# Kernel tuning notes

Measured on AMD Instinct MI355X. Metric: run time of the kernel, lower is better.

The kernel has to match this reference:

```python
import jax, jax.numpy as jnp
import numpy as np

V = 32000; EMB = 128; EH = 256; DH = 256; AD = 256; BN = 512
UNK, START, END, PAD = 0, 1, 2, 3
COV_FACTOR = 1.0
B, T_IN, T_TGT = 16, 400, 100


def _lstm_cell(x, h, c, Wih, Whh, b):
    # PyTorch gate order: i, f, g, o
    g = x @ Wih.T + h @ Whh.T + b
    i, f, gg, o = jnp.split(g, 4, axis=-1)
    c = jax.nn.sigmoid(f) * c + jax.nn.sigmoid(i) * jnp.tanh(gg)
    h = jax.nn.sigmoid(o) * jnp.tanh(c)
    return h, c


def _lstm_scan(xs, Wih, Whh, b):
    # xs: [T, B, Din]
    Bz, H = xs.shape[1], Whh.shape[-1]
    def step(carry, xt):
        h, c = _lstm_cell(xt, carry[0], carry[1], Wih, Whh, b)
        return (h, c), h
    init = (jnp.zeros((Bz, H), xs.dtype), jnp.zeros((Bz, H), xs.dtype))
    (hT, cT), hs = jax.lax.scan(step, init, xs)
    return hs, hT, cT


def _bilstm(x, Wih, Whh, b):
    # x: [B, T, Din]; Wih/Whh/b stacked over direction (fwd, bwd)
    xs = jnp.swapaxes(x, 0, 1)
    hf, hTf, cTf = _lstm_scan(xs, Wih[0], Whh[0], b[0])
    hb, hTb, cTb = _lstm_scan(xs[::-1], Wih[1], Whh[1], b[1])
    out = jnp.concatenate([hf, hb[::-1]], axis=-1)  # [T, B, 2H]
    return jnp.swapaxes(out, 0, 1), jnp.concatenate([hTf, hTb], -1), jnp.concatenate([cTf, cTb], -1)


def forward_loss(emb, enc_Wih0, enc_Whh0, enc_b0, enc_Wih1, enc_Whh1, enc_b1, W_e2dh, b_e2dh, W_e2dc, b_e2dc, dec_Wih0, dec_Whh0, dec_b0, dec_Wih1, dec_Whh1, dec_b1, W_enc_attn, b_enc_attn, W_dec_attn, w_cov, v_attn, W_v1, b_v1, W_v2, b_v2, w_ctx_sw, b_ctx_sw, w_dec_sw, w_emb_sw, input_ids, target_ids, target_lengths):
    Bz, Tt = target_ids.shape
    safe_in = jnp.where(input_ids >= V, UNK, input_ids)
    x0 = emb[safe_in]                                          # [B, T_in, EMB]
    h_seq, hT0, cT0 = _bilstm(x0, enc_Wih0, enc_Whh0, enc_b0)
    enc_states, hT1, cT1 = _bilstm(h_seq, enc_Wih1, enc_Whh1, enc_b1)  # [B, T_in, 2*EH]
    hT = jnp.stack([hT0, hT1])                                 # [2, B, 2*EH] (fwd||bwd per layer)
    cT = jnp.stack([cT0, cT1])
    dec_h = hT @ W_e2dh.T + b_e2dh                             # [2, B, DH]
    dec_c = cT @ W_e2dc.T + b_e2dc
    enc_attn = enc_states @ W_enc_attn.T + b_enc_attn          # precomputed, loop-invariant
    pad_mask = input_ids == PAD
    safe_tgt = jnp.where(target_ids >= V, UNK, target_ids)
    # teacher forcing: input at t=0 is <s>, then safe(target[t-1])
    tok_in = jnp.concatenate([jnp.full((Bz, 1), START, dtype=target_ids.dtype), safe_tgt[:, :-1]], axis=1)

    def step(carry, inp):
        dh, dc, coverage, nll, cov = carry
        tok_t, tgt_t, t = inp
        e = emb[tok_t]
        h0, c0 = _lstm_cell(e, dh[0], dc[0], dec_Wih0, dec_Whh0, dec_b0)
        h1, c1 = _lstm_cell(h0, dh[1], dc[1], dec_Wih1, dec_Whh1, dec_b1)
        feat = jnp.tanh(enc_attn + (h1 @ W_dec_attn.T)[:, None, :] + coverage[..., None] * w_cov)
        scores = jnp.where(pad_mask, -jnp.inf, feat @ v_attn)
        attn = jax.nn.softmax(scores, axis=1)                  # [B, T_in]
        ctx = jnp.einsum('bt,btd->bd', attn, enc_states)
        vd = jax.nn.softmax(jax.nn.relu(jnp.concatenate([h1, ctx], axis=1) @ W_v1.T + b_v1) @ W_v2.T + b_v2, axis=1)
        # extended vocab = END left-pad zeros + generation dist (max_num_oovs = 0)
        p_vocab = jnp.take_along_axis(jnp.pad(vd, ((0, 0), (END, 0))), tgt_t[:, None], axis=1)[:, 0]
        p_gen = jax.nn.sigmoid(ctx @ w_ctx_sw + b_ctx_sw[0] + h1 @ w_dec_sw + e @ w_emb_sw)
        p_copy = jnp.sum(attn * (input_ids == tgt_t[:, None]), axis=1)
        p = p_gen * p_vocab + (1.0 - p_gen) * p_copy
        active = t < target_lengths
        nll = nll - jnp.where(active, jnp.log(p + 1e-9), 0.0)
        cov = cov + jnp.where(active, jnp.sum(jnp.minimum(attn, coverage), axis=1), 0.0)
        return (jnp.stack([h0, h1]), jnp.stack([c0, c1]), coverage + attn, nll, cov), None

    init = (dec_h, dec_c, jnp.zeros(input_ids.shape, enc_states.dtype), jnp.zeros((Bz,), enc_states.dtype), jnp.zeros((Bz,), enc_states.dtype))
    (_, _, _, nll, cov), _ = jax.lax.scan(step, init, (tok_in.T, target_ids.T, jnp.arange(Tt)))
    nll_loss = nll.sum()
    cov_loss = cov.sum()
    return jnp.stack([nll_loss, cov_loss, nll_loss + COV_FACTOR * cov_loss])


def setup_inputs() -> dict:
    ks = iter(jax.random.split(jax.random.key(0), 48))
    def w(shape, scale=0.05):
        return (jax.random.normal(next(ks), shape) * scale).astype(jnp.float32)
    def lstm_b(*shape):
        b = np.zeros(shape, np.float32)
        n = shape[-1]
        b[..., n // 4: n // 2] = 1.0  # forget-gate bias = 1 as in init_weights
        return jnp.asarray(b)
    inp = {}
    inp['batch_input_ids'] = jax.random.randint(next(ks), (B, T_IN), 0, V)
    inp['batch_target_ids'] = jax.random.randint(next(ks), (B, T_TGT), 0, V)
    inp['input_lengths'] = jnp.full((B,), T_IN, dtype=jnp.int32)  # full-length batch
    inp['target_lengths'] = jax.random.randint(next(ks), (B,), 1, T_TGT + 1)
    inp['emb'] = w((V, EMB), 0.1)
    inp['enc_Wih0'] = w((2, 4 * EH, EMB)); inp['enc_Whh0'] = w((2, 4 * EH, EH)); inp['enc_b0'] = lstm_b(2, 4 * EH)
    inp['enc_Wih1'] = w((2, 4 * EH, 2 * EH)); inp['enc_Whh1'] = w((2, 4 * EH, EH)); inp['enc_b1'] = lstm_b(2, 4 * EH)
    inp['W_e2dh'] = w((DH, 2 * EH)); inp['b_e2dh'] = jnp.zeros((DH,), jnp.float32)
    inp['W_e2dc'] = w((DH, 2 * EH)); inp['b_e2dc'] = jnp.zeros((DH,), jnp.float32)
    inp['dec_Wih0'] = w((4 * DH, EMB)); inp['dec_Whh0'] = w((4 * DH, DH)); inp['dec_b0'] = lstm_b(4 * DH)
    inp['dec_Wih1'] = w((4 * DH, DH)); inp['dec_Whh1'] = w((4 * DH, DH)); inp['dec_b1'] = lstm_b(4 * DH)
    inp['W_enc_attn'] = w((AD, 2 * EH)); inp['b_enc_attn'] = jnp.zeros((AD,), jnp.float32)
    inp['W_dec_attn'] = w((AD, DH))
    inp['w_cov'] = w((AD,))
    inp['v_attn'] = w((AD,))
    inp['W_v1'] = w((BN, DH + 2 * EH)); inp['b_v1'] = jnp.zeros((BN,), jnp.float32)
    inp['W_v2'] = w((V - END, BN)); inp['b_v2'] = jnp.zeros((V - END,), jnp.float32)
    inp['w_ctx_sw'] = w((2 * EH,)); inp['b_ctx_sw'] = jnp.zeros((1,), jnp.float32)
    inp['w_dec_sw'] = w((DH,)); inp['w_emb_sw'] = w((EMB,))
    return inp


def reference(batch_input_ids, batch_target_ids, input_lengths, target_lengths, emb, enc_Wih0, enc_Whh0, enc_b0, enc_Wih1, enc_Whh1, enc_b1, W_e2dh, b_e2dh, W_e2dc, b_e2dc, dec_Wih0, dec_Whh0, dec_b0, dec_Wih1, dec_Whh1, dec_b1, W_enc_attn, b_enc_attn, W_dec_attn, w_cov, v_attn, W_v1, b_v1, W_v2, b_v2, w_ctx_sw, b_ctx_sw, w_dec_sw, w_emb_sw):
    del input_lengths  # all sequences are full length -> pack/pad_packed is identity
    return forward_loss(emb, enc_Wih0, enc_Whh0, enc_b0, enc_Wih1, enc_Whh1, enc_b1, W_e2dh, b_e2dh, W_e2dc, b_e2dc, dec_Wih0, dec_Whh0, dec_b0, dec_Wih1, dec_Whh1, dec_b1, W_enc_attn, b_enc_attn, W_dec_attn, w_cov, v_attn, W_v1, b_v1, W_v2, b_v2, w_ctx_sw, b_ctx_sw, w_dec_sw, w_emb_sw, batch_input_ids, batch_target_ids, target_lengths)
```

## Files before the change

### kernel.cpp

```cpp
#include <hip/hip_runtime.h>
#include <hip/hip_bf16.h>

#define B    16
#define TIN  400
#define TT   100
#define EMBD 128
#define VV   32000
#define NV   31998
#define NVB  192
#define NB   256
#define LR   112
#define REP  8

__device__ __forceinline__ float sigf(float x) { return 1.f / (1.f + __expf(-x)); }
__device__ __forceinline__ float fast_tanh(float x) {
    float e = __expf(2.f * x);
    return 1.f - 2.f / (e + 1.f);
}
__device__ __forceinline__ float bflo(unsigned u) { return __uint_as_float(u << 16); }
__device__ __forceinline__ float bfhi(unsigned u) { return __uint_as_float(u & 0xffff0000u); }
__device__ __forceinline__ float bfu(unsigned short u) { return __uint_as_float((unsigned)u << 16); }
__device__ __forceinline__ unsigned short f2bf(float f) {
    unsigned u = __float_as_uint(f);
    return (unsigned short)((u + 0x7fffu + ((u >> 16) & 1u)) >> 16);
}
__device__ __forceinline__ float cldf(const float* p) {
    return __hip_atomic_load(p, __ATOMIC_RELAXED, __HIP_MEMORY_SCOPE_AGENT);
}
__device__ __forceinline__ unsigned cldu(const unsigned* p) {
    return __hip_atomic_load(p, __ATOMIC_RELAXED, __HIP_MEMORY_SCOPE_AGENT);
}
__device__ __forceinline__ unsigned long long cldu2(const unsigned long long* p) {
    return __hip_atomic_load(p, __ATOMIC_RELAXED, __HIP_MEMORY_SCOPE_AGENT);
}
__device__ __forceinline__ void stf(float* p, float v) {
    __hip_atomic_store(p, v, __ATOMIC_RELAXED, __HIP_MEMORY_SCOPE_AGENT);
}
__device__ __forceinline__ void stu(unsigned* p, unsigned v) {
    __hip_atomic_store(p, v, __ATOMIC_RELAXED, __HIP_MEMORY_SCOPE_AGENT);
}

template<int SLP>
__device__ __forceinline__ void wait_np(int* arr, int n, int ep, int tid) {
    for (int i = tid; i < n; i += 256) {
        while (__hip_atomic_load(&arr[i * 16], __ATOMIC_RELAXED, __HIP_MEMORY_SCOPE_AGENT) < ep)
            __builtin_amdgcn_s_sleep(SLP);
    }
    __syncthreads();
    asm volatile("" ::: "memory");
}
template<int SLP>
__device__ __forceinline__ void wait_line(int* l, int ep) {
    if (threadIdx.x == 0) {
        while (__hip_atomic_load(l, __ATOMIC_RELAXED, __HIP_MEMORY_SCOPE_AGENT) < ep)
            __builtin_amdgcn_s_sleep(SLP);
    }
    __syncthreads();
    asm volatile("" ::: "memory");
}
__device__ __forceinline__ void arrive(int* arr, int idx, int ep) {
    __syncthreads();
    if (threadIdx.x == 0)
        __hip_atomic_store(&arr[idx * 16], ep, __ATOMIC_RELEASE, __HIP_MEMORY_SCOPE_AGENT);
}

__global__ __launch_bounds__(256) void k_zero(float* __restrict__ p, int n) {
    int i = blockIdx.x * 256 + threadIdx.x;
    if (i < n) p[i] = 0.f;
}

__global__ __launch_bounds__(256) void k_cvt(const float* __restrict__ src, unsigned short* __restrict__ dst, int n) {
    int i = blockIdx.x * 256 + threadIdx.x;
    if (i < n) dst[i] = f2bf(src[i]);
}

__global__ __launch_bounds__(256) void k_gx0(const int* __restrict__ ids, const float* __restrict__ emb,
                                             const float* __restrict__ Wih, const float* __restrict__ bias,
                                             float* __restrict__ gx) {
    int blk = blockIdx.x, dir = blk / TIN, t = blk % TIN;
    __shared__ float se[16][132];
    int tid = threadIdx.x;
    for (int i = tid; i < 16 * 128; i += 256) {
        int b = i >> 7, k = i & 127;
        int id = ids[b * TIN + t];
        if ((unsigned)id >= VV) id = 0;
        se[b][k] = emb[(size_t)id * EMBD + k];
    }
    __syncthreads();
    const float* W = Wih + (size_t)dir * 1024 * EMBD;
    const float* bb = bias + (size_t)dir * 1024;
    float* out = gx + ((size_t)dir * TIN + t) * (B * 1024);
    for (int c = tid; c < 1024; c += 256) {
        float acc[16];
#pragma unroll
        for (int b = 0; b < 16; b++) acc[b] = 0.f;
        const float4* wr = (const float4*)(W + (size_t)c * EMBD);
        for (int k4 = 0; k4 < 32; k4++) {
            float4 w = wr[k4];
            int k = k4 * 4;
#pragma unroll
            for (int b = 0; b < 16; b++)
                acc[b] += w.x * se[b][k] + w.y * se[b][k + 1] + w.z * se[b][k + 2] + w.w * se[b][k + 3];
        }
        float bv = bb[c];
#pragma unroll
        for (int b = 0; b < 16; b++) out[(size_t)b * 1024 + c] = acc[b] + bv;
    }
}

__global__ __launch_bounds__(256) void k_gx1(const float* __restrict__ hseq, const float* __restrict__ Wih,
                                             const float* __restrict__ bias, float* __restrict__ gx) {
    int blk = blockIdx.x, dir = blk / TIN, t = blk % TIN;
    __shared__ float sx[16][516];
    int tid = threadIdx.x;
    for (int i = tid; i < 16 * 512; i += 256) sx[i >> 9][i & 511] = hseq[(size_t)t * B * 512 + i];
    __syncthreads();
    const float* W = Wih + (size_t)dir * 1024 * 512;
    const float* bb = bias + (size_t)dir * 1024;
    float* out = gx + ((size_t)dir * TIN + t) * (B * 1024);
    for (int c = tid; c < 1024; c += 256) {
        float acc[16];
#pragma unroll
        for (int b = 0; b < 16; b++) acc[b] = 0.f;
        const float4* wr = (const float4*)(W + (size_t)c * 512);
        for (int k4 = 0; k4 < 128; k4++) {
            float4 w = wr[k4];
            int k = k4 * 4;
#pragma unroll
            for (int b = 0; b < 16; b++)
                acc[b] += w.x * sx[b][k] + w.y * sx[b][k + 1] + w.z * sx[b][k + 2] + w.w * sx[b][k + 3];
        }
        float bv = bb[c];
#pragma unroll
        for (int b = 0; b < 16; b++) out[(size_t)b * 1024 + c] = acc[b] + bv;
    }
}

__global__ __launch_bounds__(256) void k_enc_layer(const float* __restrict__ gx, const float* __restrict__ Whh,
                                                   float* __restrict__ hbuf, float* __restrict__ hout,
                                                   float* __restrict__ hTs, float* __restrict__ cTs,
                                                   int* __restrict__ slots, int layer) {
    int blk = blockIdx.x;
    int dir = blk >> 4;
    int ublk = blk & 15;
    int tid = threadIdx.x;
    int rp = tid >> 3, q = tid & 7;
    int lr0 = rp * 2, lr1 = lr0 + 1;
    int g0 = lr0 & 3, g1 = lr1 & 3;
    int unit0 = ublk * 16 + (lr0 >> 2);
    int unit1 = ublk * 16 + (lr1 >> 2);
    const float* Wd = Whh + (size_t)dir * 1024 * 256;
    float wreg[64];
    {
        const float* r0 = Wd + (size_t)(g0 * 256 + unit0) * 256 + q * 32;
        const float* r1 = Wd + (size_t)(g1 * 256 + unit1) * 256 + q * 32;
#pragma unroll
        for (int e = 0; e < 32; e++) { wreg[e] = r0[e]; wreg[32 + e] = r1[e]; }
    }
    int ub = tid >> 4, bb = tid & 15;
    float creg = 0.f;
    __shared__ float sh[16 * 288];
    __shared__ float sums[32 * 17];
    __shared__ float sums2[32 * 17];
    int* dirslots = slots + (size_t)dir * TIN * 16 * 16;

    for (int s = 0; s < TIN; s++) {
        int t = dir ? (TIN - 1 - s) : s;
        int par = s & 1;
        {
            const unsigned long long* hp = (const unsigned long long*)(hbuf + ((size_t)par * 2 + dir) * B * 256);
            unsigned long long v[8];
#pragma unroll
            for (int j = 0; j < 8; j++) v[j] = cldu2(hp + tid + 256 * j);
#pragma unroll
            for (int j = 0; j < 8; j++) {
                int k2 = (tid + 256 * j) * 2;
                int b = k2 >> 8, k = k2 & 255;
                float* d = &sh[b * 288 + (k >> 5) * 36 + (k & 31)];
                d[0] = __uint_as_float((unsigned)v[j]);
                d[1] = __uint_as_float((unsigned)(v[j] >> 32));
            }
        }
        __syncthreads();
        float pa0[16], pa1[16];
        for (int b = 0; b < 16; b++) {
            const float4* hv = (const float4*)&sh[b * 288 + q * 36];
            float a0 = 0.f, a1 = 0.f;
#pragma unroll
            for (int j = 0; j < 8; j++) {
                float4 h4 = hv[j];
                a0 += wreg[4 * j] * h4.x + wreg[4 * j + 1] * h4.y + wreg[4 * j + 2] * h4.z + wreg[4 * j + 3] * h4.w;
                a1 += wreg[32 + 4 * j] * h4.x + wreg[33 + 4 * j] * h4.y + wreg[34 + 4 * j] * h4.z + wreg[35 + 4 * j] * h4.w;
            }
            pa0[b] = a0; pa1[b] = a1;
        }
#pragma unroll
        for (int m = 1; m < 8; m <<= 1) {
#pragma unroll
            for (int b = 0; b < 16; b++) {
                pa0[b] += __shfl_xor(pa0[b], m, 64);
                pa1[b] += __shfl_xor(pa1[b], m, 64);
            }
        }
        if (q == 0) {
            float* s0 = (lr0 < 32) ? sums : sums2;
            float* s1 = (lr1 < 32) ? sums : sums2;
            int l0 = lr0 & 31, l1 = lr1 & 31;
#pragma unroll
            for (int b = 0; b < 16; b++) { s0[l0 * 17 + b] = pa0[b]; s1[l1 * 17 + b] = pa1[b]; }
        }
        __syncthreads();
        {
            int unit = ublk * 16 + ub;
            const float* gp = gx + (((size_t)dir * TIN + t) * B + bb) * 1024;
            int lri = ub * 4;
            float ai = ((lri + 0 < 32) ? sums[(lri + 0) * 17 + bb] : sums2[((lri + 0) & 31) * 17 + bb]) + gp[0 * 256 + unit];
            float af = ((lri + 1 < 32) ? sums[(lri + 1) * 17 + bb] : sums2[((lri + 1) & 31) * 17 + bb]) + gp[1 * 256 + unit];
            float ag = ((lri + 2 < 32) ? sums[(lri + 2) * 17 + bb] : sums2[((lri + 2) & 31) * 17 + bb]) + gp[2 * 256 + unit];
            float ao = ((lri + 3 < 32) ? sums[(lri + 3) * 17 + bb] : sums2[((lri + 3) & 31) * 17 + bb]) + gp[3 * 256 + unit];
            float c = sigf(af) * creg + sigf(ai) * fast_tanh(ag);
            float h = sigf(ao) * fast_tanh(c);
            creg = c;
            stf(&hbuf[((size_t)(par ^ 1) * 2 + dir) * B * 256 + (size_t)bb * 256 + unit], h);
            if (layer == 0) hout[((size_t)t * B + bb) * 512 + dir * 256 + unit] = h;
            else            hout[((size_t)bb * TIN + t) * 512 + dir * 256 + unit] = h;
            if (s == TIN - 1) {
                hTs[((size_t)layer * B + bb) * 512 + dir * 256 + unit] = h;
                cTs[((size_t)layer * B + bb) * 512 + dir * 256 + unit] = c;
            }
        }
        int* sl = dirslots + (size_t)s * 16 * 16;
        arrive(sl, ublk, 1);
        wait_np<2>(sl, 16, 1, tid);
    }
}

__global__ __launch_bounds__(256) void k_encattn(const float* __restrict__ encs, const float* __restrict__ Wea,
                                                 const float* __restrict__ bea, unsigned short* __restrict__ encat) {
    int blk = blockIdx.x;
    __shared__ float sx[8][520];
    int tid = threadIdx.x;
    for (int i = tid; i < 8 * 512; i += 256) {
        int r = i >> 9, k = i & 511;
        sx[r][k] = encs[((size_t)blk * 8 + r) * 512 + k];
    }
    __syncthreads();
    float a[8];
    float bv = bea[tid];
#pragma unroll
    for (int r = 0; r < 8; r++) a[r] = bv;
    const float4* wr = (const float4*)(Wea + (size_t)tid * 512);
    for (int k4 = 0; k4 < 128; k4++) {
        float4 w = wr[k4];
        int k = k4 * 4;
#pragma unroll
        for (int r = 0; r < 8; r++)
            a[r] += w.x * sx[r][k] + w.y * sx[r][k + 1] + w.z * sx[r][k + 2] + w.w * sx[r][k + 3];
    }
#pragma unroll
    for (int r = 0; r < 8; r++)
        encat[((size_t)blk * 8 + r) * 256 + tid] = f2bf(a[r]);
}

__global__ __launch_bounds__(256) void k_dec_init(const float* __restrict__ hTs, const float* __restrict__ cTs,
                                                  const float* __restrict__ Wh, const float* __restrict__ bh,
                                                  const float* __restrict__ Wc, const float* __restrict__ bc,
                                                  float* __restrict__ h0s, float* __restrict__ c0,
                                                  float* __restrict__ h1s, float* __restrict__ c1) {
    int idx = blockIdx.x * 256 + threadIdx.x;
    int l = idx >> 12, b = (idx >> 8) & 15, d = idx & 255;
    const float4* h4 = (const float4*)(hTs + ((size_t)l * B + b) * 512);
    const float4* c4 = (const float4*)(cTs + ((size_t)l * B + b) * 512);
    const float4* wh4 = (const float4*)(Wh + (size_t)d * 512);
    const float4* wc4 = (const float4*)(Wc + (size_t)d * 512);
    float ah = bh[d], ac = bc[d];
    for (int k4 = 0; k4 < 128; k4++) {
        float4 w = wh4[k4], x = h4[k4];
        ah += w.x * x.x + w.y * x.y + w.z * x.z + w.w * x.w;
        w = wc4[k4]; x = c4[k4];
        ac += w.x * x.x + w.y * x.y + w.z * x.z + w.w * x.w;
    }
    if (l == 0) { h0s[(size_t)b * 256 + d] = ah; c0[(size_t)b * 256 + d] = ac; }
    else        { h1s[(size_t)b * 256 + d] = ah; c1[(size_t)b * 256 + d] = ac; }
}

__global__ __launch_bounds__(256, 1) void k_dec_persist(
    const int* __restrict__ ids, const int* __restrict__ tgt, const int* __restrict__ tlen,
    const float* __restrict__ emb,
    const float* __restrict__ dWih0, const float* __restrict__ dWhh0, const float* __restrict__ db0,
    const float* __restrict__ dWih1, const float* __restrict__ dWhh1, const float* __restrict__ db1,
    const float* __restrict__ Wda, const float* __restrict__ wcov, const float* __restrict__ vat,
    const float* __restrict__ Wv1, const float* __restrict__ bv1,
    const unsigned short* __restrict__ W2b, const float* __restrict__ bv2,
    const float* __restrict__ wctx, const float* __restrict__ bctx,
    const float* __restrict__ wdec, const float* __restrict__ wemb,
    const unsigned short* __restrict__ ENCATH, const unsigned short* __restrict__ ENCSH,
    float* __restrict__ COVL,
    unsigned* __restrict__ CTXB, unsigned* __restrict__ FC1B,
    float* __restrict__ PCOPYR, float* __restrict__ VPARTR, float* __restrict__ LTGTR,
    float* __restrict__ H0R, const float* __restrict__ C0i,
    float* __restrict__ H1R, const float* __restrict__ C1i,
    int* __restrict__ SL, float* __restrict__ out)
{
    __shared__ float smem[39040];
    int blk = blockIdx.x, tid = threadIdx.x;
    int* B1 = SL;
    int* B2 = SL + 32 * 16;
    int* B3 = SL + 64 * 16;
    int* B4 = SL + 80 * 16;
    int* SVOC = SL + 96 * 16;
    int* SFRDY = SL + 288 * 16;
    int* FINRDY = SL + 296 * 16;

    if (blk < 32) {
        float creg0 = 0.f, creg1 = 0.f;
        if (tid < 128) {
            creg0 = C0i[(size_t)(tid & 15) * 256 + blk * 8 + (tid >> 4)];
            creg1 = C1i[(size_t)(tid & 15) * 256 + blk * 8 + (tid >> 4)];
        }
        for (int t = 0; t < TT; t++) {
            int ep = t + 1, p8 = t & 7, pm = (t + 7) & 7;
            wait_line<8>(FINRDY, t - 7);
            wait_np<2>(B2, 32, t, tid);

            for (int i = tid; i < 2048; i += 256) {
                int b = i >> 7, k = i & 127;
                int tok = (t == 0) ? 1 : tgt[b * TT + t - 1];
                if ((unsigned)tok >= VV) tok = 0;
                smem[b * 132 + k] = emb[(size_t)tok * 128 + k];
            }
            {
                const unsigned long long* s0 = (const unsigned long long*)(H0R + (size_t)pm * 4096);
                const unsigned long long* s1 = (const unsigned long long*)(H1R + (size_t)pm * 4096);
                unsigned long long v0[8], v1[8];
#pragma unroll
                for (int j = 0; j < 8; j++) v0[j] = cldu2(s0 + tid + 256 * j);
#pragma unroll
                for (int j = 0; j < 8; j++) v1[j] = cldu2(s1 + tid + 256 * j);
#pragma unroll
                for (int j = 0; j < 8; j++) {
                    int k2 = (tid + 256 * j) * 2;
                    int b = k2 >> 8, k = k2 & 255;
                    int off = b * 288 + (k >> 5) * 36 + (k & 31);
                    smem[2112 + off] = __uint_as_float((unsigned)v0[j]);
                    smem[2113 + off] = __uint_as_float((unsigned)(v0[j] >> 32));
                    smem[6720 + off] = __uint_as_float((unsigned)v1[j]);
                    smem[6721 + off] = __uint_as_float((unsigned)(v1[j] >> 32));
                }
            }
            __syncthreads();
            {
                int r = tid >> 3, q = tid & 7;
                int g = r & 3, u = r >> 2;
                int grow = g * 256 + blk * 8 + u;
                float4 wA[4], wB[8];
                const float4* wi4 = (const float4*)(dWih0 + (size_t)grow * 128 + q * 16);
                const float4* wh4 = (const float4*)(dWhh0 + (size_t)grow * 256 + q * 32);
#pragma unroll
                for (int j = 0; j < 4; j++) wA[j] = wi4[j];
#pragma unroll
                for (int j = 0; j < 8; j++) wB[j] = wh4[j];
                float pa[16];
                for (int b = 0; b < 16; b++) {
                    const float4* xe = (const float4*)&smem[b * 132 + q * 16];
                    const float4* xh = (const float4*)&smem[2112 + b * 288 + q * 36];
                    float a = 0.f;
#pragma unroll
                    for (int j = 0; j < 4; j++) { float4 x = xe[j]; a += wA[j].x * x.x + wA[j].y * x.y + wA[j].z * x.z + wA[j].w * x.w; }
#pragma unroll
                    for (int j = 0; j < 8; j++) { float4 x = xh[j]; a += wB[j].x * x.x + wB[j].y * x.y + wB[j].z * x.z + wB[j].w * x.w; }
                    pa[b] = a;
                }
#pragma unroll
                for (int m = 1; m < 8; m <<= 1)
#pragma unroll
                    for (int b = 0; b < 16; b++) pa[b] += __shfl_xor(pa[b], m, 64);
                if (q == 0)
#pragma unroll
                    for (int b = 0; b < 16; b++) smem[11328 + r * 17 + b] = pa[b];
            }
            __syncthreads();
            if (tid < 128) {
                int u = tid >> 4, b = tid & 15;
                int unit = blk * 8 + u;
                float ai = smem[11328 + (u * 4 + 0) * 17 + b] + db0[unit];
                float af = smem[11328 + (u * 4 + 1) * 17 + b] + db0[256 + unit];
                float ag = smem[11328 + (u * 4 + 2) * 17 + b] + db0[512 + unit];
                float ao = smem[11328 + (u * 4 + 3) * 17 + b] + db0[768 + unit];
                float c = sigf(af) * creg0 + sigf(ai) * fast_tanh(ag);
                float h = sigf(ao) * fast_tanh(c);
                creg0 = c;
                stf(&H0R[(size_t)p8 * 4096 + b * 256 + unit], h);
            }
            arrive(B1, blk, ep);
            wait_np<2>(B1, 32, ep, tid);
            {
                const unsigned long long* s0 = (const unsigned long long*)(H0R + (size_t)p8 * 4096);
                unsigned long long v0[8];
#pragma unroll
                for (int j = 0; j < 8; j++) v0[j] = cldu2(s0 + tid + 256 * j);
#pragma unroll
                for (int j = 0; j < 8; j++) {
                    int k2 = (tid + 256 * j) * 2;
                    int b = k2 >> 8, k = k2 & 255;
                    int off = b * 288 + (k >> 5) * 36 + (k & 31);
                    smem[2112 + off] = __uint_as_float((unsigned)v0[j]);
                    smem[2113 + off] = __uint_as_float((unsigned)(v0[j] >> 32));
                }
            }
            __syncthreads();
            {
                int r = tid >> 3, q = tid & 7;
                int g = r & 3, u = r >> 2;
                int grow = g * 256 + blk * 8 + u;
                float4 wA[8], wB[8];
                const float4* wi4 = (const float4*)(dWih1 + (size_t)grow * 256 + q * 32);
                const float4* wh4 = (const float4*)(dWhh1 + (size_t)grow * 256 + q * 32);
#pragma unroll
                for (int j = 0; j < 8; j++) { wA[j] = wi4[j]; wB[j] = wh4[j]; }
                float pa[16];
                for (int b = 0; b < 16; b++) {
                    const float4* xa = (const float4*)&smem[2112 + b * 288 + q * 36];
                    const float4* xb = (const float4*)&smem[6720 + b * 288 + q * 36];
                    float a = 0.f;
#pragma unroll
                    for (int j = 0; j < 8; j++) { float4 x = xa[j]; a += wA[j].x * x.x + wA[j].y * x.y + wA[j].z * x.z + wA[j].w * x.w; }
#pragma unroll
                    for (int j = 0; j < 8; j++) { float4 x = xb[j]; a += wB[j].x * x.x + wB[j].y * x.y + wB[j].z * x.z + wB[j].w * x.w; }
                    pa[b] = a;
                }
#pragma unroll
                for (int m = 1; m < 8; m <<= 1)
#pragma unroll
                    for (int b = 0; b < 16; b++) pa[b] += __shfl_xor(pa[b], m, 64);
                if (q == 0)
#pragma unroll
                    for (int b = 0; b < 16; b++) smem[11328 + r * 17 + b] = pa[b];
            }
            __syncthreads();
            if (tid < 128) {
                int u = tid >> 4, b = tid & 15;
                int unit = blk * 8 + u;
                float ai = smem[11328 + (u * 4 + 0) * 17 + b] + db1[unit];
                float af = smem[11328 + (u * 4 + 1) * 17 + b] + db1[256 + unit];
                float ag = smem[11328 + (u * 4 + 2) * 17 + b] + db1[512 + unit];
                float ao = smem[11328 + (u * 4 + 3) * 17 + b] + db1[768 + unit];
                float c = sigf(af) * creg1 + sigf(ai) * fast_tanh(ag);
                float h = sigf(ao) * fast_tanh(c);
                creg1 = c;
                stf(&H1R[(size_t)p8 * 4096 + b * 256 + unit], h);
            }
            arrive(B2, blk, ep);
        }
    } else if (blk < 48) {
        int b = blk - 32;
        float* sh1 = smem; float* sda = smem + 256; float* ssc = smem + 512;
        float* red = smem + 912; float* sred = smem + 1280; float* scov = smem + 3328;
        for (int i = tid; i < TIN; i += 256) scov[i] = 0.f;
        float covl = 0.f;
        __syncthreads();
        for (int t = 0; t < TT; t++) {
            int ep = t + 1, p8 = t & 7;
            wait_np<2>(B2, 32, ep, tid);
            if (tid < 128) {
                unsigned long long v = cldu2((const unsigned long long*)(H1R + (size_t)p8 * 4096 + b * 256) + tid);
                sh1[2 * tid] = __uint_as_float((unsigned)v);
                sh1[2 * tid + 1] = __uint_as_float((unsigned)(v >> 32));
            }
            __syncthreads();
            {
                float a = 0.f;
                const float4* wr = (const float4*)(Wda + (size_t)tid * 256);
                const float4* h4 = (const float4*)sh1;
                for (int k4 = 0; k4 < 64; k4++) {
                    float4 ww = wr[k4], x = h4[k4];
                    a += ww.x * x.x + ww.y * x.y + ww.z * x.z + ww.w * x.w;
                }
                sda[tid] = a;
            }
            __syncthreads();
            int lane = tid & 63, wv = tid >> 6;
            for (int tt = wv; tt < TIN; tt += 4) {
                float cvv = scov[tt];
                const unsigned short* ea = ENCATH + ((size_t)b * TIN + tt) * 256;
                float s4 = 0.f;
#pragma unroll
                for (int j = 0; j < 4; j++) {
                    int c = lane + 64 * j;
                    float x = bfu(ea[c]) + sda[c] + cvv * wcov[c];
                    s4 += vat[c] * fast_tanh(x);
                }
#pragma unroll
                for (int o = 32; o > 0; o >>= 1) s4 += __shfl_xor(s4, o, 64);
                if (lane == 0) ssc[tt] = (ids[b * TIN + tt] == 3) ? -1e30f : s4;
            }
            __syncthreads();
            float m = -1e30f;
            for (int i = tid; i < TIN; i += 256) m = fmaxf(m, ssc[i]);
            red[tid] = m; __syncthreads();
            for (int o = 128; o > 0; o >>= 1) { if (tid < o) red[tid] = fmaxf(red[tid], red[tid + o]); __syncthreads(); }
            m = red[0]; __syncthreads();
            float ps = 0.f;
            for (int i = tid; i < TIN; i += 256) { float ex = __expf(ssc[i] - m); ssc[i] = ex; ps += ex; }
            red[tid] = ps; __syncthreads();
            for (int o = 128; o > 0; o >>= 1) { if (tid < o) red[tid] += red[tid + o]; __syncthreads(); }
            float inv = 1.f / red[0];
            __syncthreads();
            int tgb = tgt[b * TT + t];
            float pc = 0.f, ca = 0.f;
            for (int i = tid; i < TIN; i += 256) {
                float at = ssc[i] * inv; ssc[i] = at;
                float cv = scov[i];
                ca += fminf(at, cv);
                scov[i] = cv + at;
                if (ids[b * TIN + i] == tgb) pc += at;
            }
            red[tid] = pc; __syncthreads();
            for (int o = 128; o > 0; o >>= 1) { if (tid < o) red[tid] += red[tid + o]; __syncthreads(); }
            if (tid == 0) stf(&PCOPYR[p8 * 16 + b], red[0]);
            __syncthreads();
            red[tid] = ca; __syncthreads();
            for (int o = 128; o > 0; o >>= 1) { if (tid < o) red[tid] += red[tid + o]; __syncthreads(); }
            if (tid == 0 && t < tlen[b]) covl += red[0];
            __syncthreads();
            {
                float acc[8];
#pragma unroll
                for (int j = 0; j < 8; j++) acc[j] = 0.f;
                for (int i = wv; i < TIN; i += 4) {
                    float a = ssc[i];
                    const unsigned short* es = ENCSH + ((size_t)b * TIN + i) * 512;
#pragma unroll
                    for (int j = 0; j < 8; j++) acc[j] += a * bfu(es[lane + 64 * j]);
                }
#pragma unroll
                for (int j = 0; j < 8; j++) sred[wv * 512 + 64 * j + lane] = acc[j];
                __syncthreads();
                {
                    int d2 = tid;
                    float c0 = sred[2 * d2] + sred[512 + 2 * d2] + sred[1024 + 2 * d2] + sred[1536 + 2 * d2];
                    float c1 = sred[2 * d2 + 1] + sred[512 + 2 * d2 + 1] + sred[1024 + 2 * d2 + 1] + sred[1536 + 2 * d2 + 1];
                    unsigned u = (unsigned)f2bf(c0) | ((unsigned)f2bf(c1) << 16);
                    stu(&CTXB[(size_t)p8 * 4096 + b * 256 + d2], u);
                }
            }
            if (t == TT - 1 && tid == 0) stf(&COVL[b], covl);
            arrive(B3, b, ep);
        }
    } else if (blk < 64) {
        int cb = blk - 48;
        float* Wv1s = smem;
        float* x = smem + 24576;
        float* fcout = smem + 36928;
        for (int r = 0; r < 32; r++)
            for (int k = tid; k < 768; k += 256)
                Wv1s[r * 768 + k] = Wv1[(size_t)(cb * 32 + r) * 768 + k];
        __syncthreads();
        for (int t = 0; t < TT; t++) {
            int ep = t + 1, p8 = t & 7;
            wait_np<2>(B3, 16, ep, tid);
            {
                const unsigned long long* s0 = (const unsigned long long*)(H1R + (size_t)p8 * 4096);
                unsigned long long v0[8];
#pragma unroll
                for (int j = 0; j < 8; j++) v0[j] = cldu2(s0 + tid + 256 * j);
#pragma unroll
                for (int j = 0; j < 8; j++) {
                    int k2 = (tid + 256 * j) * 2;
                    int b = k2 >> 8, k = k2 & 255;
                    x[b * 772 + k] = __uint_as_float((unsigned)v0[j]);
                    x[b * 772 + k + 1] = __uint_as_float((unsigned)(v0[j] >> 32));
                }
                const unsigned long long* s1 = (const unsigned long long*)(CTXB + (size_t)p8 * 4096);
                unsigned long long w1[8];
#pragma unroll
                for (int j = 0; j < 8; j++) w1[j] = cldu2(s1 + tid + 256 * j);
#pragma unroll
                for (int j = 0; j < 8; j++) {
                    int g = (tid + 256 * j) * 2;
                    int b = g >> 8, pj = g & 255;
                    unsigned lo = (unsigned)w1[j], hi = (unsigned)(w1[j] >> 32);
                    float* d = &x[b * 772 + 256 + 2 * pj];
                    d[0] = bflo(lo); d[1] = bfhi(lo); d[2] = bflo(hi); d[3] = bfhi(hi);
                }
            }
            __syncthreads();
            {
                int b = tid & 15, cl = tid >> 4;
                const float4* xr = (const float4*)&x[b * 772];
#pragma unroll
                for (int half = 0; half < 2; half++) {
                    int lc = half * 16 + cl;
                    float a = bv1[cb * 32 + lc];
                    const float4* wr = (const float4*)&Wv1s[lc * 768];
                    for (int k4 = 0; k4 < 192; k4++) {
                        float4 ww = wr[k4], xx = xr[k4];
                        a += ww.x * xx.x + ww.y * xx.y + ww.z * xx.z + ww.w * xx.w;
                    }
                    fcout[b * 32 + lc] = fmaxf(a, 0.f);
                }
            }
            __syncthreads();
            {
                int bb = tid >> 4, j = tid & 15;
                unsigned u = (unsigned)f2bf(fcout[bb * 32 + 2 * j]) | ((unsigned)f2bf(fcout[bb * 32 + 2 * j + 1]) << 16);
#pragma unroll
                for (int rp = 0; rp < REP; rp++)
                    stu(&FC1B[((size_t)rp * 8 + p8) * 4096 + bb * 256 + cb * 16 + j], u);
            }
            arrive(B4, cb, ep);
            if (blk == 63) {
                wait_np<2>(B4, 16, ep, tid);
                if (tid == 0) {
#pragma unroll
                    for (int rp = 0; rp < REP; rp++)
                        __hip_atomic_store(&SFRDY[rp * 16], ep, __ATOMIC_RELEASE, __HIP_MEMORY_SCOPE_AGENT);
                }
                __syncthreads();
            }
        }
    } else {
        int vb = blk - 64;
        int start = (int)(((long long)vb * NV) / NVB);
        int end   = (int)(((long long)(vb + 1) * NV) / NVB);
        float* FC1f = smem + 28672;
        float* scratch = smem + 36864;
        uint4* Wl = (uint4*)smem;
        const unsigned* myFC1B = FC1B + (size_t)(vb & 7) * 8 * 4096;
        int* mySF = &SFRDY[(vb & 7) * 16];
        float nllreg = 0.f;
        for (int i = tid; i < LR * 64; i += 256) {
            int row = i >> 6, k8 = i & 63;
            Wl[k8 * LR + row] = *(const uint4*)(W2b + (size_t)(start + row) * 512 + k8 * 8);
        }
        __syncthreads();

        for (int t = 0; t < TT; t++) {
            int ep = t + 1, p8 = t & 7;
            wait_line<4>(mySF, ep);
            {
                const unsigned long long* src = (const unsigned long long*)(myFC1B + (size_t)p8 * 4096);
                unsigned long long v[8];
#pragma unroll
                for (int j = 0; j < 8; j++) v[j] = cldu2(src + tid + 256 * j);
#pragma unroll
                for (int j = 0; j < 8; j++) {
                    int iu = tid + 256 * j;
                    unsigned lo = (unsigned)v[j], hi = (unsigned)(v[j] >> 32);
                    *(float4*)&FC1f[iu * 4] = make_float4(bflo(lo), bfhi(lo), bflo(hi), bfhi(hi));
                }
            }
            __syncthreads();
            int vl = tid & 127, kh = tid >> 7;
            float esum[16];
#pragma unroll
            for (int b = 0; b < 16; b++) esum[b] = 0.f;
            for (int chunk = 0; chunk < 2; chunk++) {
                int v = (chunk == 0) ? (start + vl) : (start + LR + vl);
                bool row_ok = (chunk == 0) ? (vl < LR) : (v < end);
                float acc[16];
#pragma unroll
                for (int b = 0; b < 16; b++) acc[b] = 0.f;
                if (row_ok) {
                    for (int k8l = 0; k8l < 32; k8l++) {
                        int k8 = kh * 32 + k8l;
                        uint4 pw = (chunk == 0) ? Wl[k8 * LR + vl]
                                                : *(const uint4*)(W2b + (size_t)v * 512 + k8 * 8);
                        int k = k8 * 8;
                        float w0 = bflo(pw.x), w1 = bfhi(pw.x);
                        float w2 = bflo(pw.y), w3 = bfhi(pw.y);
                        float w4 = bflo(pw.z), w5 = bfhi(pw.z);
                        float w6 = bflo(pw.w), w7 = bfhi(pw.w);
#pragma unroll
                        for (int b = 0; b < 16; b++) {
                            const float* s = &FC1f[b * 512 + k];
                            acc[b] += w0 * s[0] + w1 * s[1] + w2 * s[2] + w3 * s[3]
                                    + w4 * s[4] + w5 * s[5] + w6 * s[6] + w7 * s[7];
                        }
                    }
                }
                if (kh == 1 && row_ok) {
#pragma unroll
                    for (int b = 0; b < 16; b++) scratch[vl * 17 + b] = acc[b];
                }
                __syncthreads();
                if (kh == 0 && row_ok) {
                    float bias = bv2[v];
#pragma unroll
                    for (int b = 0; b < 16; b++) {
                        float lg = acc[b] + scratch[vl * 17 + b] + bias;
                        if (tgt[b * TT + t] - 2 == v) stf(&LTGTR[p8 * 16 + b], lg);
                        esum[b] += __expf(lg);
                    }
                }
                __syncthreads();
            }
            if (kh == 0) {
#pragma unroll
                for (int b = 0; b < 16; b++) scratch[vl * 17 + b] = esum[b];
            }
            __syncthreads();
            {
                int b = tid >> 4, sl = tid & 15;
                float s = 0.f;
#pragma unroll
                for (int j = 0; j < 8; j++) s += scratch[(sl + 16 * j) * 17 + b];
                FC1f[b * 17 + sl] = s;
            }
            __syncthreads();
            if (tid < 16) {
                float den = 0.f;
#pragma unroll
                for (int j = 0; j < 16; j++) den += FC1f[tid * 17 + j];
                stf(&VPARTR[(size_t)p8 * 3072 + tid * 192 + vb], den);
            }
            __syncthreads();
            arrive(SVOC, vb, ep);

            if (blk == NB - 1) {
                wait_np<2>(SVOC, NVB, ep, tid);
                float* fsc = FC1f;
                int lane = tid & 63, wv = tid >> 6;
                for (int bi = 0; bi < 4; bi++) {
                    int b = wv * 4 + bi;
                    float a = 0.f;
                    for (int k = lane; k < 256; k += 64) {
                        unsigned u = cldu(&CTXB[(size_t)p8 * 4096 + b * 256 + k]);
                        a += bflo(u) * wctx[2 * k] + bfhi(u) * wctx[2 * k + 1];
                    }
                    for (int k = lane; k < 256; k += 64) a += cldf(&H1R[(size_t)p8 * 4096 + b * 256 + k]) * wdec[k];
                    int tok = (t == 0) ? 1 : tgt[b * TT + t - 1];
                    if ((unsigned)tok >= VV) tok = 0;
                    const float* em = emb + (size_t)tok * EMBD;
                    for (int k = lane; k < 128; k += 64) a += em[k] * wemb[k];
#pragma unroll
                    for (int o = 32; o > 0; o >>= 1) a += __shfl_xor(a, o, 64);
                    if (lane == 0) fsc[300 + b] = a;
                }
                {
                    int b = tid >> 4, sl = tid & 15;
                    float s = 0.f;
                    for (int j = sl; j < NVB; j += 16) s += cldf(&VPARTR[(size_t)p8 * 3072 + b * 192 + j]);
                    fsc[b * 17 + sl] = s;
                }
                __syncthreads();
                if (tid < 16) {
                    int b = tid;
                    float den = 0.f;
#pragma unroll
                    for (int j = 0; j < 16; j++) den += fsc[b * 17 + j];
                    float pg = 1.f / (1.f + __expf(-(fsc[300 + b] + bctx[0])));
                    int tg = tgt[b * TT + t];
                    float pv = (tg >= 2) ? (__expf(cldf(&LTGTR[p8 * 16 + b])) / den) : 0.f;
                    float pr = pg * pv + (1.f - pg) * cldf(&PCOPYR[p8 * 16 + b]);
                    if (t < tlen[b]) nllreg += -logf(pr + 1e-9f);
                }
                if (t == TT - 1) {
                    if (tid < 16) fsc[340 + tid] = nllreg;
                    __syncthreads();
                    if (tid == 0) {
                        float sn = 0.f, sc = 0.f;
                        for (int b = 0; b < 16; b++) { sn += fsc[340 + b]; sc += cldf(&COVL[b]); }
                        out[0] = sn; out[1] = sc; out[2] = sn + sc;
                    }
                }
                __syncthreads();
                if (tid == 0)
                    __hip_atomic_store(FINRDY, ep, __ATOMIC_RELEASE, __HIP_MEMORY_SCOPE_AGENT);
            }
        }
    }
}

extern "C" void kernel_launch(void* const* d_in, const int* in_sizes, int n_in,
                              void* d_out, int out_size, void* d_ws, size_t ws_size,
                              hipStream_t stream) {
    (void)in_sizes; (void)n_in; (void)out_size; (void)ws_size;
    const int*   ids   = (const int*)d_in[0];
    const int*   tgt   = (const int*)d_in[1];
    const int*   tlen  = (const int*)d_in[3];
    const float* emb   = (const float*)d_in[4];
    const float* eWih0 = (const float*)d_in[5];
    const float* eWhh0 = (const float*)d_in[6];
    const float* eb0   = (const float*)d_in[7];
    const float* eWih1 = (const float*)d_in[8];
    const float* eWhh1 = (const float*)d_in[9];
    const float* eb1   = (const float*)d_in[10];
    const float* We2dh = (const float*)d_in[11];
    const float* be2dh = (const float*)d_in[12];
    const float* We2dc = (const float*)d_in[13];
    const float* be2dc = (const float*)d_in[14];
    const float* dWih0 = (const float*)d_in[15];
    const float* dWhh0 = (const float*)d_in[16];
    const float* db0   = (const float*)d_in[17];
    const float* dWih1 = (const float*)d_in[18];
    const float* dWhh1 = (const float*)d_in[19];
    const float* db1   = (const float*)d_in[20];
    const float* Wea   = (const float*)d_in[21];
    const float* bea   = (const float*)d_in[22];
    const float* Wda   = (const float*)d_in[23];
    const float* wcov  = (const float*)d_in[24];
    const float* vat   = (const float*)d_in[25];
    const float* Wv1   = (const float*)d_in[26];
    const float* bv1   = (const float*)d_in[27];
    const float* Wv2   = (const float*)d_in[28];
    const float* bv2   = (const float*)d_in[29];
    const float* wctx  = (const float*)d_in[30];
    const float* bctx  = (const float*)d_in[31];
    const float* wdec  = (const float*)d_in[32];
    const float* wemb  = (const float*)d_in[33];
    float* out = (float*)d_out;

    float* ws = (float*)d_ws;
    float* GX    = ws; ws += (size_t)2 * TIN * B * 1024;
    float* HSEQ  = ws; ws += (size_t)TIN * B * 512;
    float* ENCS  = ws; ws += (size_t)B * TIN * 512;
    float* ENCATHf = ws; ws += (size_t)B * TIN * 128;
    float* ENCSHf  = ws; ws += (size_t)B * TIN * 256;
    float* HTS   = ws; ws += 2 * B * 512;
    float* CTS   = ws; ws += 2 * B * 512;
    float* H0R   = ws; ws += 8 * B * 256;
    float* C0    = ws; ws += B * 256;
    float* H1R   = ws; ws += 8 * B * 256;
    float* C1    = ws; ws += B * 256;
    float* CTXBf = ws; ws += 8 * 4096;
    float* FC1Bf = ws; ws += (size_t)REP * 8 * 4096;
    float* PCOPYR= ws; ws += 8 * B;
    float* VPARTR= ws; ws += (size_t)8 * B * NVB;
    float* LTGTR = ws; ws += 8 * B;
    float* COVL  = ws; ws += B;
    float* ZBASE = ws;
    float* EHBUF = ws; ws += 2 * 2 * B * 256;
    float* ENCSL0f = ws; ws += (size_t)2 * TIN * 16 * 16;
    float* ENCSL1f = ws; ws += (size_t)2 * TIN * 16 * 16;
    float* SLf     = ws; ws += 304 * 16;
    int zcount = (int)(ws - ZBASE);

    int* ENCSL0 = (int*)ENCSL0f;
    int* ENCSL1 = (int*)ENCSL1f;
    int* SLp    = (int*)SLf;
    unsigned short* WV2B = (unsigned short*)GX;
    unsigned short* ENCATH = (unsigned short*)ENCATHf;
    unsigned short* ENCSH  = (unsigned short*)ENCSHf;
    unsigned* CTXB = (unsigned*)CTXBf;
    unsigned* FC1B = (unsigned*)FC1Bf;

    k_zero<<<(zcount + 255) / 256, 256, 0, stream>>>(ZBASE, zcount);
    k_gx0<<<2 * TIN, 256, 0, stream>>>(ids, emb, eWih0, eb0, GX);
    k_enc_layer<<<32, 256, 0, stream>>>(GX, eWhh0, EHBUF, HSEQ, HTS, CTS, ENCSL0, 0);
    k_gx1<<<2 * TIN, 256, 0, stream>>>(HSEQ, eWih1, eb1, GX);
    k_zero<<<64, 256, 0, stream>>>(EHBUF, 2 * 2 * B * 256);
    k_enc_layer<<<32, 256, 0, stream>>>(GX, eWhh1, EHBUF, ENCS, HTS, CTS, ENCSL1, 1);
    k_cvt<<<(NV * 512 + 255) / 256, 256, 0, stream>>>(Wv2, WV2B, NV * 512);
    k_cvt<<<(B * TIN * 512 + 255) / 256, 256, 0, stream>>>(ENCS, ENCSH, B * TIN * 512);
    k_encattn<<<B * TIN / 8, 256, 0, stream>>>(ENCS, Wea, bea, ENCATH);
    k_dec_init<<<32, 256, 0, stream>>>(HTS, CTS, We2dh, be2dh, We2dc, be2dc,
                                       H0R + (size_t)7 * B * 256, C0,
                                       H1R + (size_t)7 * B * 256, C1);
    k_dec_persist<<<NB, 256, 0, stream>>>(ids, tgt, tlen, emb,
                                          dWih0, dWhh0, db0, dWih1, dWhh1, db1,
                                          Wda, wcov, vat, Wv1, bv1, WV2B, bv2,
                                          wctx, bctx, wdec, wemb,
                                          ENCATH, ENCSH, COVL, CTXB, FC1B,
                                          PCOPYR, VPARTR, LTGTR, H0R, C0, H1R, C1, SLp, out);
}
```

Baseline: 16.19 ms.

## Restructure decoder persistent kernel: per-batch LSTM blocks, bf16 weights, deeper ring buffers

Replaces the 32-block grid-synchronized decoder LSTM with 16 blocks that each run one batch row through both layers independently. The LSTM and FC1 weights are pre-packed into bf16. The ring depth grows from 8 to 16 so stages can run further ahead, and the vocab block count is raised. Hidden states are exchanged as packed bf16, and FC1 data goes through a relay with explicit cache-bypassing loads. This removes per-step cross-block barriers, at the cost of redundant weight reads per batch block and extra bf16 precision loss.

```diff
diff --git a/kernel.cpp b/kernel.cpp
--- a/kernel.cpp
+++ b/kernel.cpp
@@ -7,10 +7,11 @@
 #define EMBD 128
 #define VV   32000
 #define NV   31998
-#define NVB  192
+#define NVB  224
 #define NB   256
 #define LR   112
-#define REP  8
+
+typedef unsigned uint4v __attribute__((ext_vector_type(4)));
 
 __device__ __forceinline__ float sigf(float x) { return 1.f / (1.f + __expf(-x)); }
 __device__ __forceinline__ float fast_tanh(float x) {
@@ -19,10 +20,12 @@
 }
 __device__ __forceinline__ float bflo(unsigned u) { return __uint_as_float(u << 16); }
 __device__ __forceinline__ float bfhi(unsigned u) { return __uint_as_float(u & 0xffff0000u); }
-__device__ __forceinline__ float bfu(unsigned short u) { return __uint_as_float((unsigned)u << 16); }
 __device__ __forceinline__ unsigned short f2bf(float f) {
     unsigned u = __float_as_uint(f);
     return (unsigned short)((u + 0x7fffu + ((u >> 16) & 1u)) >> 16);
+}
+__device__ __forceinline__ unsigned packbf(float a, float b) {
+    return (unsigned)f2bf(a) | ((unsigned)f2bf(b) << 16);
 }
 __device__ __forceinline__ float cldf(const float* p) {
     return __hip_atomic_load(p, __ATOMIC_RELAXED, __HIP_MEMORY_SCOPE_AGENT);
@@ -72,6 +75,18 @@
 __global__ __launch_bounds__(256) void k_cvt(const float* __restrict__ src, unsigned short* __restrict__ dst, int n) {
     int i = blockIdx.x * 256 + threadIdx.x;
     if (i < n) dst[i] = f2bf(src[i]);
+}
+
+__global__ __launch_bounds__(256) void k_pack(const float* __restrict__ A, int wA,
+                                              const float* __restrict__ Bw, int wB,
+                                              unsigned short* __restrict__ dst, int rows) {
+    int i = blockIdx.x * 256 + threadIdx.x;
+    int W = wA + wB;
+    if (i < rows * W) {
+        int r = i / W, k = i - r * W;
+        float v = (k < wA) ? A[(size_t)r * wA + k] : Bw[(size_t)r * wB + (k - wA)];
+        dst[i] = f2bf(v);
+    }
 }
 
 __global__ __launch_bounds__(256) void k_gx0(const int* __restrict__ ids, const float* __restrict__ emb,
@@ -136,6 +151,19 @@
     }
 }
 
+__device__ __forceinline__ void slot_signal_e(int* sl, int idx) {
+    __syncthreads();
+    if (threadIdx.x == 0)
+        __hip_atomic_store(&sl[idx * 16], 1, __ATOMIC_RELEASE, __HIP_MEMORY_SCOPE_AGENT);
+}
+__device__ __forceinline__ void slot_wait_e(int* sl, int n, int tid) {
+    for (int i = tid; i < n; i += 256) {
+        while (__hip_atomic_load(&sl[i * 16], __ATOMIC_RELAXED, __HIP_MEMORY_SCOPE_AGENT) == 0)
+            __builtin_amdgcn_s_sleep(2);
+    }
+    __syncthreads();
+    asm volatile("" ::: "memory");
+}
 __global__ __launch_bounds__(256) void k_enc_layer(const float* __restrict__ gx, const float* __restrict__ Whh,
                                                    float* __restrict__ hbuf, float* __restrict__ hout,
                                                    float* __restrict__ hTs, float* __restrict__ cTs,
@@ -230,8 +258,8 @@
             }
         }
         int* sl = dirslots + (size_t)s * 16 * 16;
-        arrive(sl, ublk, 1);
-        wait_np<2>(sl, 16, 1, tid);
+        slot_signal_e(sl, ublk);
+        slot_wait_e(sl, 16, tid);
     }
 }
 
@@ -287,185 +315,136 @@
 __global__ __launch_bounds__(256, 1) void k_dec_persist(
     const int* __restrict__ ids, const int* __restrict__ tgt, const int* __restrict__ tlen,
     const float* __restrict__ emb,
-    const float* __restrict__ dWih0, const float* __restrict__ dWhh0, const float* __restrict__ db0,
-    const float* __restrict__ dWih1, const float* __restrict__ dWhh1, const float* __restrict__ db1,
+    const unsigned short* __restrict__ CW0B, const float* __restrict__ db0,
+    const unsigned short* __restrict__ CW1B, const float* __restrict__ db1,
     const float* __restrict__ Wda, const float* __restrict__ wcov, const float* __restrict__ vat,
-    const float* __restrict__ Wv1, const float* __restrict__ bv1,
+    const unsigned short* __restrict__ WV1B, const float* __restrict__ bv1,
     const unsigned short* __restrict__ W2b, const float* __restrict__ bv2,
     const float* __restrict__ wctx, const float* __restrict__ bctx,
     const float* __restrict__ wdec, const float* __restrict__ wemb,
     const unsigned short* __restrict__ ENCATH, const unsigned short* __restrict__ ENCSH,
     float* __restrict__ COVL,
-    unsigned* __restrict__ CTXB, unsigned* __restrict__ FC1B,
+    unsigned* __restrict__ H1B, unsigned* __restrict__ CTXB,
+    unsigned* __restrict__ FC1B, unsigned* __restrict__ RELAY,
     float* __restrict__ PCOPYR, float* __restrict__ VPARTR, float* __restrict__ LTGTR,
-    float* __restrict__ H0R, const float* __restrict__ C0i,
-    float* __restrict__ H1R, const float* __restrict__ C1i,
+    const float* __restrict__ H0I, const float* __restrict__ C0i,
+    const float* __restrict__ H1I, const float* __restrict__ C1i,
     int* __restrict__ SL, float* __restrict__ out)
 {
     __shared__ float smem[39040];
     int blk = blockIdx.x, tid = threadIdx.x;
-    int* B1 = SL;
-    int* B2 = SL + 32 * 16;
-    int* B3 = SL + 64 * 16;
-    int* B4 = SL + 80 * 16;
-    int* SVOC = SL + 96 * 16;
-    int* SFRDY = SL + 288 * 16;
-    int* FINRDY = SL + 296 * 16;
-
-    if (blk < 32) {
-        float creg0 = 0.f, creg1 = 0.f;
-        if (tid < 128) {
-            creg0 = C0i[(size_t)(tid & 15) * 256 + blk * 8 + (tid >> 4)];
-            creg1 = C1i[(size_t)(tid & 15) * 256 + blk * 8 + (tid >> 4)];
-        }
+    int* CELLRDY = SL;
+    int* ATTNRDY = SL + 16 * 16;
+    int* SVOC    = SL + 32 * 16;
+    int* RELAYRDY= SL + 256 * 16;
+    int* FINRDY  = SL + 264 * 16;
+    int* CLAIM   = SL + 272 * 16;
+
+    if (blk < 16) {
+        int b = blk, u = tid;
+        float* xemb = smem;
+        float* h0 = smem + 128;
+        float* h1 = smem + 384;
+        float c0reg = C0i[b * 256 + u];
+        float c1reg = C1i[b * 256 + u];
+        h0[u] = H0I[b * 256 + u];
+        h1[u] = H1I[b * 256 + u];
+        __syncthreads();
         for (int t = 0; t < TT; t++) {
-            int ep = t + 1, p8 = t & 7, pm = (t + 7) & 7;
-            wait_line<8>(FINRDY, t - 7);
-            wait_np<2>(B2, 32, t, tid);
-
-            for (int i = tid; i < 2048; i += 256) {
-                int b = i >> 7, k = i & 127;
-                int tok = (t == 0) ? 1 : tgt[b * TT + t - 1];
-                if ((unsigned)tok >= VV) tok = 0;
-                smem[b * 132 + k] = emb[(size_t)tok * 128 + k];
+            int p16 = t & 15;
+            wait_line<8>(FINRDY, t - 15);
+            int tok = (t == 0) ? 1 : tgt[b * TT + t - 1];
+            if ((unsigned)tok >= VV) tok = 0;
+            if (tid < 128) xemb[tid] = emb[(size_t)tok * 128 + tid];
+            __syncthreads();
+            float acc0[4];
+#pragma unroll
+            for (int g = 0; g < 4; g++) {
+                const uint4* wr = (const uint4*)CW0B + (size_t)(g * 256 + u) * 48;
+                float a = 0.f;
+                for (int i = 0; i < 16; i++) {
+                    uint4 q = wr[i]; int k = i * 8;
+                    a += bflo(q.x) * xemb[k]     + bfhi(q.x) * xemb[k + 1]
+                       + bflo(q.y) * xemb[k + 2] + bfhi(q.y) * xemb[k + 3]
+                       + bflo(q.z) * xemb[k + 4] + bfhi(q.z) * xemb[k + 5]
+                       + bflo(q.w) * xemb[k + 6] + bfhi(q.w) * xemb[k + 7];
+                }
+                for (int i = 16; i < 48; i++) {
+                    uint4 q = wr[i]; int k = i * 8 - 128;
+                    a += bflo(q.x) * h0[k]     + bfhi(q.x) * h0[k + 1]
+                       + bflo(q.y) * h0[k + 2] + bfhi(q.y) * h0[k + 3]
+                       + bflo(q.z) * h0[k + 4] + bfhi(q.z) * h0[k + 5]
+                       + bflo(q.w) * h0[k + 6] + bfhi(q.w) * h0[k + 7];
+                }
+                acc0[g] = a;
             }
             {
-                const unsigned long long* s0 = (const unsigned long long*)(H0R + (size_t)pm * 4096);
-                const unsigned long long* s1 = (const unsigned long long*)(H1R + (size_t)pm * 4096);
-                unsigned long long v0[8], v1[8];
-#pragma unroll
-                for (int j = 0; j < 8; j++) v0[j] = cldu2(s0 + tid + 256 * j);
-#pragma unroll
-                for (int j = 0; j < 8; j++) v1[j] = cldu2(s1 + tid + 256 * j);
-#pragma unroll
-                for (int j = 0; j < 8; j++) {
-                    int k2 = (tid + 256 * j) * 2;
-                    int b = k2 >> 8, k = k2 & 255;
-                    int off = b * 288 + (k >> 5) * 36 + (k & 31);
-                    smem[2112 + off] = __uint_as_float((unsigned)v0[j]);
-                    smem[2113 + off] = __uint_as_float((unsigned)(v0[j] >> 32));
-                    smem[6720 + off] = __uint_as_float((unsigned)v1[j]);
-                    smem[6721 + off] = __uint_as_float((unsigned)(v1[j] >> 32));
-                }
-            }
-            __syncthreads();
+                float ai = acc0[0] + db0[u], af = acc0[1] + db0[256 + u];
+                float ag = acc0[2] + db0[512 + u], ao = acc0[3] + db0[768 + u];
+                float c = sigf(af) * c0reg + sigf(ai) * fast_tanh(ag);
+                float h = sigf(ao) * fast_tanh(c);
+                c0reg = c;
+                __syncthreads();
+                h0[u] = h;
+            }
+            __syncthreads();
+            float acc1[4];
+#pragma unroll
+            for (int g = 0; g < 4; g++) {
+                const uint4* wr = (const uint4*)CW1B + (size_t)(g * 256 + u) * 64;
+                float a = 0.f;
+                for (int i = 0; i < 32; i++) {
+                    uint4 q = wr[i]; int k = i * 8;
+                    a += bflo(q.x) * h0[k]     + bfhi(q.x) * h0[k + 1]
+                       + bflo(q.y) * h0[k + 2] + bfhi(q.y) * h0[k + 3]
+                       + bflo(q.z) * h0[k + 4] + bfhi(q.z) * h0[k + 5]
+                       + bflo(q.w) * h0[k + 6] + bfhi(q.w) * h0[k + 7];
+                }
+                for (int i = 32; i < 64; i++) {
+                    uint4 q = wr[i]; int k = i * 8 - 256;
+                    a += bflo(q.x) * h1[k]     + bfhi(q.x) * h1[k + 1]
+                       + bflo(q.y) * h1[k + 2] + bfhi(q.y) * h1[k + 3]
+                       + bflo(q.z) * h1[k + 4] + bfhi(q.z) * h1[k + 5]
+                       + bflo(q.w) * h1[k + 6] + bfhi(q.w) * h1[k + 7];
+                }
+                acc1[g] = a;
+            }
             {
-                int r = tid >> 3, q = tid & 7;
-                int g = r & 3, u = r >> 2;
-                int grow = g * 256 + blk * 8 + u;
-                float4 wA[4], wB[8];
-                const float4* wi4 = (const float4*)(dWih0 + (size_t)grow * 128 + q * 16);
-                const float4* wh4 = (const float4*)(dWhh0 + (size_t)grow * 256 + q * 32);
-#pragma unroll
-                for (int j = 0; j < 4; j++) wA[j] = wi4[j];
-#pragma unroll
-                for (int j = 0; j < 8; j++) wB[j] = wh4[j];
-                float pa[16];
-                for (int b = 0; b < 16; b++) {
-                    const float4* xe = (const float4*)&smem[b * 132 + q * 16];
-                    const float4* xh = (const float4*)&smem[2112 + b * 288 + q * 36];
-                    float a = 0.f;
-#pragma unroll
-                    for (int j = 0; j < 4; j++) { float4 x = xe[j]; a += wA[j].x * x.x + wA[j].y * x.y + wA[j].z * x.z + wA[j].w * x.w; }
-#pragma unroll
-                    for (int j = 0; j < 8; j++) { float4 x = xh[j]; a += wB[j].x * x.x + wB[j].y * x.y + wB[j].z * x.z + wB[j].w * x.w; }
-                    pa[b] = a;
-                }
-#pragma unroll
-                for (int m = 1; m < 8; m <<= 1)
-#pragma unroll
-                    for (int b = 0; b < 16; b++) pa[b] += __shfl_xor(pa[b], m, 64);
-                if (q == 0)
-#pragma unroll
-                    for (int b = 0; b < 16; b++) smem[11328 + r * 17 + b] = pa[b];
-            }
-            __syncthreads();
-            if (tid < 128) {
-                int u = tid >> 4, b = tid & 15;
-                int unit = blk * 8 + u;
-                float ai = smem[11328 + (u * 4 + 0) * 17 + b] + db0[unit];
-                float af = smem[11328 + (u * 4 + 1) * 17 + b] + db0[256 + unit];
-                float ag = smem[11328 + (u * 4 + 2) * 17 + b] + db0[512 + unit];
-                float ao = smem[11328 + (u * 4 + 3) * 17 + b] + db0[768 + unit];
-                float c = sigf(af) * creg0 + sigf(ai) * fast_tanh(ag);
+                float ai = acc1[0] + db1[u], af = acc1[1] + db1[256 + u];
+                float ag = acc1[2] + db1[512 + u], ao = acc1[3] + db1[768 + u];
+                float c = sigf(af) * c1reg + sigf(ai) * fast_tanh(ag);
                 float h = sigf(ao) * fast_tanh(c);
-                creg0 = c;
-                stf(&H0R[(size_t)p8 * 4096 + b * 256 + unit], h);
-            }
-            arrive(B1, blk, ep);
-            wait_np<2>(B1, 32, ep, tid);
-            {
-                const unsigned long long* s0 = (const unsigned long long*)(H0R + (size_t)p8 * 4096);
-                unsigned long long v0[8];
-#pragma unroll
-                for (int j = 0; j < 8; j++) v0[j] = cldu2(s0 + tid + 256 * j);
-#pragma unroll
-                for (int j = 0; j < 8; j++) {
-                    int k2 = (tid + 256 * j) * 2;
-                    int b = k2 >> 8, k = k2 & 255;
-                    int off = b * 288 + (k >> 5) * 36 + (k & 31);
-                    smem[2112 + off] = __uint_as_float((unsigned)v0[j]);
-                    smem[2113 + off] = __uint_as_float((unsigned)(v0[j] >> 32));
-                }
-            }
-            __syncthreads();
-            {
-                int r = tid >> 3, q = tid & 7;
-                int g = r & 3, u = r >> 2;
-                int grow = g * 256 + blk * 8 + u;
-                float4 wA[8], wB[8];
-                const float4* wi4 = (const float4*)(dWih1 + (size_t)grow * 256 + q * 32);
-                const float4* wh4 = (const float4*)(dWhh1 + (size_t)grow * 256 + q * 32);
-#pragma unroll
-                for (int j = 0; j < 8; j++) { wA[j] = wi4[j]; wB[j] = wh4[j]; }
-                float pa[16];
-                for (int b = 0; b < 16; b++) {
-                    const float4* xa = (const float4*)&smem[2112 + b * 288 + q * 36];
-                    const float4* xb = (const float4*)&smem[6720 + b * 288 + q * 36];
-                    float a = 0.f;
-#pragma unroll
-                    for (int j = 0; j < 8; j++) { float4 x = xa[j]; a += wA[j].x * x.x + wA[j].y * x.y + wA[j].z * x.z + wA[j].w * x.w; }
-#pragma unroll
-                    for (int j = 0; j < 8; j++) { float4 x = xb[j]; a += wB[j].x * x.x + wB[j].y * x.y + wB[j].z * x.z + wB[j].w * x.w; }
-                    pa[b] = a;
-                }
-#pragma unroll
-                for (int m = 1; m < 8; m <<= 1)
-#pragma unroll
-                    for (int b = 0; b < 16; b++) pa[b] += __shfl_xor(pa[b], m, 64);
-                if (q == 0)
-#pragma unroll
-                    for (int b = 0; b < 16; b++) smem[11328 + r * 17 + b] = pa[b];
-            }
-            __syncthreads();
-            if (tid < 128) {
-                int u = tid >> 4, b = tid & 15;
-                int unit = blk * 8 + u;
-                float ai = smem[11328 + (u * 4 + 0) * 17 + b] + db1[unit];
-                float af = smem[11328 + (u * 4 + 1) * 17 + b] + db1[256 + unit];
-                float ag = smem[11328 + (u * 4 + 2) * 17 + b] + db1[512 + unit];
-                float ao = smem[11328 + (u * 4 + 3) * 17 + b] + db1[768 + unit];
-                float c = sigf(af) * creg1 + sigf(ai) * fast_tanh(ag);
-                float h = sigf(ao) * fast_tanh(c);
-                creg1 = c;
-                stf(&H1R[(size_t)p8 * 4096 + b * 256 + unit], h);
-            }
-            arrive(B2, blk, ep);
-        }
-    } else if (blk < 48) {
-        int b = blk - 32;
-        float* sh1 = smem; float* sda = smem + 256; float* ssc = smem + 512;
-        float* red = smem + 912; float* sred = smem + 1280; float* scov = smem + 3328;
+                c1reg = c;
+                __syncthreads();
+                h1[u] = h;
+            }
+            __syncthreads();
+            if (tid < 128)
+                stu(&H1B[p16 * 2048 + b * 128 + tid], packbf(h1[2 * tid], h1[2 * tid + 1]));
+            arrive(CELLRDY, b, t + 1);
+        }
+    } else if (blk < 32) {
+        int b = blk - 16;
+        float* sh1 = smem;
+        float* sda = smem + 256;
+        float* ssc = smem + 512;
+        float* red = smem + 912;
+        float* sred = smem + 1280;
+        float* scov = smem + 3328;
+        float* ctxv = smem + 3728;
+        float* fcout = smem + 4240;
         for (int i = tid; i < TIN; i += 256) scov[i] = 0.f;
         float covl = 0.f;
         __syncthreads();
         for (int t = 0; t < TT; t++) {
-            int ep = t + 1, p8 = t & 7;
-            wait_np<2>(B2, 32, ep, tid);
-            if (tid < 128) {
-                unsigned long long v = cldu2((const unsigned long long*)(H1R + (size_t)p8 * 4096 + b * 256) + tid);
-                sh1[2 * tid] = __uint_as_float((unsigned)v);
-                sh1[2 * tid + 1] = __uint_as_float((unsigned)(v >> 32));
+            int p16 = t & 15;
+            wait_line<8>(FINRDY, t - 15);
+            wait_line<2>(&CELLRDY[b * 16], t + 1);
+            if (tid < 64) {
+                unsigned long long v = cldu2((const unsigned long long*)(H1B + p16 * 2048 + b * 128) + tid);
+                unsigned lo = (unsigned)v, hi = (unsigned)(v >> 32);
+                sh1[4 * tid] = bflo(lo); sh1[4 * tid + 1] = bfhi(lo);
+                sh1[4 * tid + 2] = bflo(hi); sh1[4 * tid + 3] = bfhi(hi);
             }
             __syncthreads();
             {
@@ -487,7 +466,7 @@
 #pragma unroll
                 for (int j = 0; j < 4; j++) {
                     int c = lane + 64 * j;
-                    float x = bfu(ea[c]) + sda[c] + cvv * wcov[c];
+                    float x = __uint_as_float((unsigned)ea[c] << 16) + sda[c] + cvv * wcov[c];
                     s4 += vat[c] * fast_tanh(x);
                 }
 #pragma unroll
@@ -517,7 +496,7 @@
             }
             red[tid] = pc; __syncthreads();
             for (int o = 128; o > 0; o >>= 1) { if (tid < o) red[tid] += red[tid + o]; __syncthreads(); }
-            if (tid == 0) stf(&PCOPYR[p8 * 16 + b], red[0]);
+            if (tid == 0) stf(&PCOPYR[p16 * 16 + b], red[0]);
             __syncthreads();
             red[tid] = ca; __syncthreads();
             for (int o = 128; o > 0; o >>= 1) { if (tid < o) red[tid] += red[tid + o]; __syncthreads(); }
@@ -531,104 +510,67 @@
                     float a = ssc[i];
                     const unsigned short* es = ENCSH + ((size_t)b * TIN + i) * 512;
 #pragma unroll
-                    for (int j = 0; j < 8; j++) acc[j] += a * bfu(es[lane + 64 * j]);
+                    for (int j = 0; j < 8; j++) acc[j] += a * __uint_as_float((unsigned)es[lane + 64 * j] << 16);
                 }
 #pragma unroll
                 for (int j = 0; j < 8; j++) sred[wv * 512 + 64 * j + lane] = acc[j];
                 __syncthreads();
-                {
-                    int d2 = tid;
-                    float c0 = sred[2 * d2] + sred[512 + 2 * d2] + sred[1024 + 2 * d2] + sred[1536 + 2 * d2];
-                    float c1 = sred[2 * d2 + 1] + sred[512 + 2 * d2 + 1] + sred[1024 + 2 * d2 + 1] + sred[1536 + 2 * d2 + 1];
-                    unsigned u = (unsigned)f2bf(c0) | ((unsigned)f2bf(c1) << 16);
-                    stu(&CTXB[(size_t)p8 * 4096 + b * 256 + d2], u);
-                }
-            }
+                for (int d = tid; d < 512; d += 256)
+                    ctxv[d] = sred[d] + sred[512 + d] + sred[1024 + d] + sred[1536 + d];
+            }
+            __syncthreads();
+            if (tid < 256)
+                stu(&CTXB[p16 * 4096 + b * 256 + tid], packbf(ctxv[2 * tid], ctxv[2 * tid + 1]));
+#pragma unroll
+            for (int half = 0; half < 2; half++) {
+                int r = tid + half * 256;
+                const uint4* wr = (const uint4*)WV1B + (size_t)r * 96;
+                float a = bv1[r];
+                for (int i = 0; i < 32; i++) {
+                    uint4 q = wr[i]; int k = i * 8;
+                    a += bflo(q.x) * sh1[k]     + bfhi(q.x) * sh1[k + 1]
+                       + bflo(q.y) * sh1[k + 2] + bfhi(q.y) * sh1[k + 3]
+                       + bflo(q.z) * sh1[k + 4] + bfhi(q.z) * sh1[k + 5]
+                       + bflo(q.w) * sh1[k + 6] + bfhi(q.w) * sh1[k + 7];
+                }
+                for (int i = 32; i < 96; i++) {
+                    uint4 q = wr[i]; int k = i * 8 - 256;
+                    a += bflo(q.x) * ctxv[k]     + bfhi(q.x) * ctxv[k + 1]
+                       + bflo(q.y) * ctxv[k + 2] + bfhi(q.y) * ctxv[k + 3]
+                       + bflo(q.z) * ctxv[k + 4] + bfhi(q.z) * ctxv[k + 5]
+                       + bflo(q.w) * ctxv[k + 6] + bfhi(q.w) * ctxv[k + 7];
+                }
+                fcout[r] = fmaxf(a, 0.f);
+            }
+            __syncthreads();
+            if (tid < 256)
+                stu(&FC1B[(size_t)t * 4096 + b * 256 + tid], packbf(fcout[2 * tid], fcout[2 * tid + 1]));
             if (t == TT - 1 && tid == 0) stf(&COVL[b], covl);
-            arrive(B3, b, ep);
-        }
-    } else if (blk < 64) {
-        int cb = blk - 48;
-        float* Wv1s = smem;
-        float* x = smem + 24576;
-        float* fcout = smem + 36928;
-        for (int r = 0; r < 32; r++)
-            for (int k = tid; k < 768; k += 256)
-                Wv1s[r * 768 + k] = Wv1[(size_t)(cb * 32 + r) * 768 + k];
-        __syncthreads();
-        for (int t = 0; t < TT; t++) {
-            int ep = t + 1, p8 = t & 7;
-            wait_np<2>(B3, 16, ep, tid);
-            {
-                const unsigned long long* s0 = (const unsigned long long*)(H1R + (size_t)p8 * 4096);
-                unsigned long long v0[8];
-#pragma unroll
-                for (int j = 0; j < 8; j++) v0[j] = cldu2(s0 + tid + 256 * j);
-#pragma unroll
-                for (int j = 0; j < 8; j++) {
-                    int k2 = (tid + 256 * j) * 2;
-                    int b = k2 >> 8, k = k2 & 255;
-                    x[b * 772 + k] = __uint_as_float((unsigned)v0[j]);
-                    x[b * 772 + k + 1] = __uint_as_float((unsigned)(v0[j] >> 32));
-                }
-                const unsigned long long* s1 = (const unsigned long long*)(CTXB + (size_t)p8 * 4096);
-                unsigned long long w1[8];
-#pragma unroll
-                for (int j = 0; j < 8; j++) w1[j] = cldu2(s1 + tid + 256 * j);
-#pragma unroll
-                for (int j = 0; j < 8; j++) {
-                    int g = (tid + 256 * j) * 2;
-                    int b = g >> 8, pj = g & 255;
-                    unsigned lo = (unsigned)w1[j], hi = (unsigned)(w1[j] >> 32);
-                    float* d = &x[b * 772 + 256 + 2 * pj];
-                    d[0] = bflo(lo); d[1] = bfhi(lo); d[2] = bflo(hi); d[3] = bfhi(hi);
-                }
-            }
-            __syncthreads();
-            {
-                int b = tid & 15, cl = tid >> 4;
-                const float4* xr = (const float4*)&x[b * 772];
-#pragma unroll
-                for (int half = 0; half < 2; half++) {
-                    int lc = half * 16 + cl;
-                    float a = bv1[cb * 32 + lc];
-                    const float4* wr = (const float4*)&Wv1s[lc * 768];
-                    for (int k4 = 0; k4 < 192; k4++) {
-                        float4 ww = wr[k4], xx = xr[k4];
-                        a += ww.x * xx.x + ww.y * xx.y + ww.z * xx.z + ww.w * xx.w;
-                    }
-                    fcout[b * 32 + lc] = fmaxf(a, 0.f);
-                }
-            }
-            __syncthreads();
-            {
-                int bb = tid >> 4, j = tid & 15;
-                unsigned u = (unsigned)f2bf(fcout[bb * 32 + 2 * j]) | ((unsigned)f2bf(fcout[bb * 32 + 2 * j + 1]) << 16);
-#pragma unroll
-                for (int rp = 0; rp < REP; rp++)
-                    stu(&FC1B[((size_t)rp * 8 + p8) * 4096 + bb * 256 + cb * 16 + j], u);
-            }
-            arrive(B4, cb, ep);
-            if (blk == 63) {
-                wait_np<2>(B4, 16, ep, tid);
-                if (tid == 0) {
-#pragma unroll
-                    for (int rp = 0; rp < REP; rp++)
-                        __hip_atomic_store(&SFRDY[rp * 16], ep, __ATOMIC_RELEASE, __HIP_MEMORY_SCOPE_AGENT);
-                }
-                __syncthreads();
-            }
+            arrive(ATTNRDY, b, t + 1);
         }
     } else {
-        int vb = blk - 64;
+        int vb = blk - 32;
         int start = (int)(((long long)vb * NV) / NVB);
         int end   = (int)(((long long)(vb + 1) * NV) / NVB);
         float* FC1f = smem + 28672;
         float* scratch = smem + 36864;
         uint4* Wl = (uint4*)smem;
-        const unsigned* myFC1B = FC1B + (size_t)(vb & 7) * 8 * 4096;
-        int* mySF = &SFRDY[(vb & 7) * 16];
         float nllreg = 0.f;
+        int xcc, isrelay;
+        {
+            if (tid == 0) {
+                int x = 0;
+                asm volatile("s_getreg_b32 %0, hwreg(HW_REG_XCC_ID)" : "=s"(x));
+                x &= 7;
+                int old = atomicCAS(&CLAIM[x * 16], 0, blk + 1);
+                scratch[0] = (float)x;
+                scratch[1] = (old == 0) ? 1.f : 0.f;
+            }
+            __syncthreads();
+            xcc = (int)scratch[0];
+            isrelay = (int)scratch[1];
+            __syncthreads();
+        }
         for (int i = tid; i < LR * 64; i += 256) {
             int row = i >> 6, k8 = i & 63;
             Wl[k8 * LR + row] = *(const uint4*)(W2b + (size_t)(start + row) * 512 + k8 * 8);
@@ -636,21 +578,54 @@
         __syncthreads();
 
         for (int t = 0; t < TT; t++) {
-            int ep = t + 1, p8 = t & 7;
-            wait_line<4>(mySF, ep);
-            {
-                const unsigned long long* src = (const unsigned long long*)(myFC1B + (size_t)p8 * 4096);
+            int p16 = t & 15;
+            wait_line<8>(FINRDY, t - 15);
+            if (isrelay) {
+                wait_np<2>(ATTNRDY, 16, t + 1, tid);
+                const unsigned long long* src = (const unsigned long long*)(FC1B + (size_t)t * 4096);
+                unsigned long long* rdst = (unsigned long long*)(RELAY + (size_t)xcc * 409600 + (size_t)t * 4096);
                 unsigned long long v[8];
 #pragma unroll
                 for (int j = 0; j < 8; j++) v[j] = cldu2(src + tid + 256 * j);
 #pragma unroll
                 for (int j = 0; j < 8; j++) {
-                    int iu = tid + 256 * j;
+                    int m = tid + 256 * j;
+                    rdst[m] = v[j];
                     unsigned lo = (unsigned)v[j], hi = (unsigned)(v[j] >> 32);
-                    *(float4*)&FC1f[iu * 4] = make_float4(bflo(lo), bfhi(lo), bflo(hi), bfhi(hi));
-                }
-            }
-            __syncthreads();
+                    FC1f[4 * m] = bflo(lo); FC1f[4 * m + 1] = bfhi(lo);
+                    FC1f[4 * m + 2] = bflo(hi); FC1f[4 * m + 3] = bfhi(hi);
+                }
+                arrive(RELAYRDY, xcc, t + 1);
+            } else {
+                wait_line<2>(&RELAYRDY[xcc * 16], t + 1);
+                const uint4v* Rbase = (const uint4v*)(RELAY + (size_t)xcc * 409600 + (size_t)t * 4096);
+                uint4v q0, q1, q2, q3;
+                const uint4v* p0 = Rbase + tid;
+                const uint4v* p1 = Rbase + tid + 256;
+                const uint4v* p2 = Rbase + tid + 512;
+                const uint4v* p3 = Rbase + tid + 768;
+                asm volatile(
+                    "global_load_dwordx4 %0, %4, off sc0\n\t"
+                    "global_load_dwordx4 %1, %5, off sc0\n\t"
+                    "global_load_dwordx4 %2, %6, off sc0\n\t"
+                    "global_load_dwordx4 %3, %7, off sc0\n\t"
+                    "s_waitcnt vmcnt(0)"
+                    : "=v"(q0), "=v"(q1), "=v"(q2), "=v"(q3)
+                    : "v"(p0), "v"(p1), "v"(p2), "v"(p3)
+                    : "memory");
+#pragma unroll
+                for (int j = 0; j < 4; j++) {
+                    uint4v q = (j == 0) ? q0 : (j == 1) ? q1 : (j == 2) ? q2 : q3;
+                    int i4 = tid + 256 * j;
+#pragma unroll
+                    for (int r = 0; r < 4; r++) {
+                        unsigned uu = q[r];
+                        FC1f[8 * i4 + 2 * r] = bflo(uu);
+                        FC1f[8 * i4 + 2 * r + 1] = bfhi(uu);
+                    }
+                }
+                __syncthreads();
+            }
             int vl = tid & 127, kh = tid >> 7;
             float esum[16];
 #pragma unroll
@@ -689,7 +664,7 @@
 #pragma unroll
                     for (int b = 0; b < 16; b++) {
                         float lg = acc[b] + scratch[vl * 17 + b] + bias;
-                        if (tgt[b * TT + t] - 2 == v) stf(&LTGTR[p8 * 16 + b], lg);
+                        if (tgt[b * TT + t] - 2 == v) stf(&LTGTR[p16 * 16 + b], lg);
                         esum[b] += __expf(lg);
                     }
                 }
@@ -712,23 +687,26 @@
                 float den = 0.f;
 #pragma unroll
                 for (int j = 0; j < 16; j++) den += FC1f[tid * 17 + j];
-                stf(&VPARTR[(size_t)p8 * 3072 + tid * 192 + vb], den);
-            }
-            __syncthreads();
-            arrive(SVOC, vb, ep);
+                stf(&VPARTR[p16 * 3584 + tid * 224 + vb], den);
+            }
+            __syncthreads();
+            arrive(SVOC, vb, t + 1);
 
             if (blk == NB - 1) {
-                wait_np<2>(SVOC, NVB, ep, tid);
+                wait_np<2>(SVOC, NVB, t + 1, tid);
                 float* fsc = FC1f;
                 int lane = tid & 63, wv = tid >> 6;
                 for (int bi = 0; bi < 4; bi++) {
                     int b = wv * 4 + bi;
                     float a = 0.f;
                     for (int k = lane; k < 256; k += 64) {
-                        unsigned u = cldu(&CTXB[(size_t)p8 * 4096 + b * 256 + k]);
+                        unsigned u = cldu(&CTXB[p16 * 4096 + b * 256 + k]);
                         a += bflo(u) * wctx[2 * k] + bfhi(u) * wctx[2 * k + 1];
                     }
-                    for (int k = lane; k < 256; k += 64) a += cldf(&H1R[(size_t)p8 * 4096 + b * 256 + k]) * wdec[k];
+                    for (int k = lane; k < 128; k += 64) {
+                        unsigned u = cldu(&H1B[p16 * 2048 + b * 128 + k]);
+                        a += bflo(u) * wdec[2 * k] + bfhi(u) * wdec[2 * k + 1];
+                    }
                     int tok = (t == 0) ? 1 : tgt[b * TT + t - 1];
                     if ((unsigned)tok >= VV) tok = 0;
                     const float* em = emb + (size_t)tok * EMBD;
@@ -740,7 +718,7 @@
                 {
                     int b = tid >> 4, sl = tid & 15;
                     float s = 0.f;
-                    for (int j = sl; j < NVB; j += 16) s += cldf(&VPARTR[(size_t)p8 * 3072 + b * 192 + j]);
+                    for (int j = sl; j < NVB; j += 16) s += cldf(&VPARTR[p16 * 3584 + b * 224 + j]);
                     fsc[b * 17 + sl] = s;
                 }
                 __syncthreads();
@@ -751,8 +729,8 @@
                     for (int j = 0; j < 16; j++) den += fsc[b * 17 + j];
                     float pg = 1.f / (1.f + __expf(-(fsc[300 + b] + bctx[0])));
                     int tg = tgt[b * TT + t];
-                    float pv = (tg >= 2) ? (__expf(cldf(&LTGTR[p8 * 16 + b])) / den) : 0.f;
-                    float pr = pg * pv + (1.f - pg) * cldf(&PCOPYR[p8 * 16 + b]);
+                    float pv = (tg >= 2) ? (__expf(cldf(&LTGTR[p16 * 16 + b])) / den) : 0.f;
+                    float pr = pg * pv + (1.f - pg) * cldf(&PCOPYR[p16 * 16 + b]);
                     if (t < tlen[b]) nllreg += -logf(pr + 1e-9f);
                 }
                 if (t == TT - 1) {
@@ -764,9 +742,7 @@
                         out[0] = sn; out[1] = sc; out[2] = sn + sc;
                     }
                 }
-                __syncthreads();
-                if (tid == 0)
-                    __hip_atomic_store(FINRDY, ep, __ATOMIC_RELEASE, __HIP_MEMORY_SCOPE_AGENT);
+                arrive(FINRDY, 0, t + 1);
             }
         }
     }
@@ -819,31 +795,36 @@
     float* ENCSHf  = ws; ws += (size_t)B * TIN * 256;
     float* HTS   = ws; ws += 2 * B * 512;
     float* CTS   = ws; ws += 2 * B * 512;
-    float* H0R   = ws; ws += 8 * B * 256;
+    float* H0I   = ws; ws += B * 256;
     float* C0    = ws; ws += B * 256;
-    float* H1R   = ws; ws += 8 * B * 256;
+    float* H1I   = ws; ws += B * 256;
     float* C1    = ws; ws += B * 256;
-    float* CTXBf = ws; ws += 8 * 4096;
-    float* FC1Bf = ws; ws += (size_t)REP * 8 * 4096;
-    float* PCOPYR= ws; ws += 8 * B;
-    float* VPARTR= ws; ws += (size_t)8 * B * NVB;
-    float* LTGTR = ws; ws += 8 * B;
-    float* COVL  = ws; ws += B;
+    float* H1Bf  = ws; ws += 16 * 2048;
+    float* CTXBf = ws; ws += 16 * 4096;
+    float* PCOPYR= ws; ws += 16 * 16;
+    float* VPARTR= ws; ws += 16 * 3584;
+    float* LTGTR = ws; ws += 16 * 16;
+    float* COVL  = ws; ws += 16;
     float* ZBASE = ws;
     float* EHBUF = ws; ws += 2 * 2 * B * 256;
     float* ENCSL0f = ws; ws += (size_t)2 * TIN * 16 * 16;
     float* ENCSL1f = ws; ws += (size_t)2 * TIN * 16 * 16;
-    float* SLf     = ws; ws += 304 * 16;
+    float* SLf     = ws; ws += 288 * 16;
     int zcount = (int)(ws - ZBASE);
 
     int* ENCSL0 = (int*)ENCSL0f;
     int* ENCSL1 = (int*)ENCSL1f;
     int* SLp    = (int*)SLf;
     unsigned short* WV2B = (unsigned short*)GX;
+    unsigned short* CW0B = (unsigned short*)(GX + 8191488);
+    unsigned short* CW1B = (unsigned short*)(GX + 8388096);
+    unsigned short* WV1B = (unsigned short*)(GX + 8650240);
+    unsigned*       FC1B = (unsigned*)(GX + 8846848);
+    unsigned*       RELAY = (unsigned*)HSEQ;
     unsigned short* ENCATH = (unsigned short*)ENCATHf;
     unsigned short* ENCSH  = (unsigned short*)ENCSHf;
+    unsigned* H1B = (unsigned*)H1Bf;
     unsigned* CTXB = (unsigned*)CTXBf;
-    unsigned* FC1B = (unsigned*)FC1Bf;
 
     k_zero<<<(zcount + 255) / 256, 256, 0, stream>>>(ZBASE, zcount);
     k_gx0<<<2 * TIN, 256, 0, stream>>>(ids, emb, eWih0, eb0, GX);
@@ -853,14 +834,15 @@
     k_enc_layer<<<32, 256, 0, stream>>>(GX, eWhh1, EHBUF, ENCS, HTS, CTS, ENCSL1, 1);
     k_cvt<<<(NV * 512 + 255) / 256, 256, 0, stream>>>(Wv2, WV2B, NV * 512);
     k_cvt<<<(B * TIN * 512 + 255) / 256, 256, 0, stream>>>(ENCS, ENCSH, B * TIN * 512);
+    k_cvt<<<(512 * 768 + 255) / 256, 256, 0, stream>>>(Wv1, WV1B, 512 * 768);
+    k_pack<<<(1024 * 384 + 255) / 256, 256, 0, stream>>>(dWih0, 128, dWhh0, 256, CW0B, 1024);
+    k_pack<<<(1024 * 512 + 255) / 256, 256, 0, stream>>>(dWih1, 256, dWhh1, 256, CW1B, 1024);
     k_encattn<<<B * TIN / 8, 256, 0, stream>>>(ENCS, Wea, bea, ENCATH);
-    k_dec_init<<<32, 256, 0, stream>>>(HTS, CTS, We2dh, be2dh, We2dc, be2dc,
-                                       H0R + (size_t)7 * B * 256, C0,
-                                       H1R + (size_t)7 * B * 256, C1);
+    k_dec_init<<<32, 256, 0, stream>>>(HTS, CTS, We2dh, be2dh, We2dc, be2dc, H0I, C0, H1I, C1);
     k_dec_persist<<<NB, 256, 0, stream>>>(ids, tgt, tlen, emb,
-                                          dWih0, dWhh0, db0, dWih1, dWhh1, db1,
-                                          Wda, wcov, vat, Wv1, bv1, WV2B, bv2,
+                                          CW0B, db0, CW1B, db1,
+                                          Wda, wcov, vat, WV1B, bv1, WV2B, bv2,
                                           wctx, bctx, wdec, wemb,
-                                          ENCATH, ENCSH, COVL, CTXB, FC1B,
-                                          PCOPYR, VPARTR, LTGTR, H0R, C0, H1R, C1, SLp, out);
-}
+                                          ENCATH, ENCSH, COVL, H1B, CTXB, FC1B, RELAY,
+                                          PCOPYR, VPARTR, LTGTR, H0I, C0, H1I, C1, SLp, out);
+}
```

Measured after the change: 20.20 ms. 1.25x slower.
